# Kernel tuning notes

Measured on AMD Instinct MI355X. Metric: run time of the kernel, lower is better.

Reference implementation:

```python
import jax, jax.numpy as jnp
import numpy as np

INPUT_SIZE = 512
HIDDEN = 1024
OUT = 512
LN_EPS = 1e-5


def setup_inputs() -> dict:
    key = jax.random.key(0)
    ks = jax.random.split(key, 12)
    B, T = 128, 512
    def lin(k, fan_in, shape):
        bound = 1.0 / np.sqrt(fan_in)
        return jax.random.uniform(k, shape, jnp.float32, -bound, bound)
    in0 = INPUT_SIZE + HIDDEN
    in1 = HIDDEN + HIDDEN
    return {
        "x": jax.random.normal(ks[0], (B, T, INPUT_SIZE), jnp.float32),
        "W0": lin(ks[1], in0, (in0, 4 * HIDDEN)),
        "b0": lin(ks[2], in0, (4 * HIDDEN,)),
        "g0": jnp.ones((4 * HIDDEN,), jnp.float32),
        "beta0": jnp.zeros((4 * HIDDEN,), jnp.float32),
        "W1": lin(ks[3], in1, (in1, 4 * HIDDEN)),
        "b1": lin(ks[4], in1, (4 * HIDDEN,)),
        "g1": jnp.ones((4 * HIDDEN,), jnp.float32),
        "beta1": jnp.zeros((4 * HIDDEN,), jnp.float32),
        "fcW": lin(ks[5], HIDDEN, (HIDDEN, OUT)),
        "fcb": lin(ks[6], HIDDEN, (OUT,)),
    }


def _layer_norm(z, g, b):
    m = jnp.mean(z, axis=-1, keepdims=True)
    v = jnp.mean((z - m) ** 2, axis=-1, keepdims=True)
    return (z - m) * jax.lax.rsqrt(v + LN_EPS) * g + b


def _cell(xin, h, c, W, b, g, beta):
    comb = jnp.concatenate([xin, h], axis=-1)          # [B, in+H]
    gates = _layer_norm(comb @ W + b, g, beta)          # [B, 4H]
    i, f, gg, o = jnp.split(gates, 4, axis=-1)
    i, f, o = jax.nn.sigmoid(i), jax.nn.sigmoid(f), jax.nn.sigmoid(o)
    gg = jnp.tanh(gg)
    c_new = f * c + i * gg
    h_new = o * jnp.tanh(c_new)
    return h_new, c_new


def reference(x, W0, b0, g0, beta0, W1, b1, g1, beta1, fcW, fcb):
    B = x.shape[0]
    params = [(W0, b0, g0, beta0), (W1, b1, g1, beta1)]
    h0 = tuple(jnp.zeros((B, HIDDEN), x.dtype) for _ in range(2))
    c0 = tuple(jnp.zeros((B, HIDDEN), x.dtype) for _ in range(2))

    def step(carry, xt):
        hs, cs = carry
        inp = xt
        new_h, new_c = [], []
        for l, (W, b, g, beta) in enumerate(params):
            hl, cl = _cell(inp, hs[l], cs[l], W, b, g, beta)
            new_h.append(hl)
            new_c.append(cl)
            inp = hl
        return (tuple(new_h), tuple(new_c)), None

    xt = jnp.swapaxes(x, 0, 1)  # [T, B, D]
    (hs, _), _ = jax.lax.scan(step, (h0, c0), xt)
    return hs[-1] @ fcW + fcb  # [B, OUT]
```

## Files before the change

### kernel.cpp

```cpp
#include <hip/hip_runtime.h>
#include <hip/hip_bf16.h>

typedef __attribute__((ext_vector_type(8))) _Float16 half8_t;
typedef __attribute__((ext_vector_type(4))) float f32x4_t;
typedef unsigned long long u64;

#define SH 2056
#define HMOFF (16 * SH)
#define LDS_BYTES (2 * 16 * SH * 2)

__device__ __forceinline__ float sigm(float z) { return 1.0f / (1.0f + __expf(-z)); }
__device__ __forceinline__ float tanh_fast(float z) {
  float e = __expf(2.0f * z);
  return 1.0f - 2.0f / (e + 1.0f);
}

__device__ __forceinline__ half8_t ld_h8_coh(const _Float16* p) {
  union { half8_t h; u64 q[2]; } r;
  u64* q = (u64*)p;
  r.q[0] = __hip_atomic_load(q,     __ATOMIC_RELAXED, __HIP_MEMORY_SCOPE_SYSTEM);
  r.q[1] = __hip_atomic_load(q + 1, __ATOMIC_RELAXED, __HIP_MEMORY_SCOPE_SYSTEM);
  return r.h;
}
__device__ __forceinline__ void st_h_coh(_Float16* p, _Float16 v) {
  unsigned short b = __builtin_bit_cast(unsigned short, v);
  __hip_atomic_store((unsigned short*)p, b, __ATOMIC_RELAXED, __HIP_MEMORY_SCOPE_SYSTEM);
}
__device__ __forceinline__ float ld_f_coh(const float* p) {
  return __hip_atomic_load((float*)p, __ATOMIC_RELAXED, __HIP_MEMORY_SCOPE_SYSTEM);
}
__device__ __forceinline__ void st_f_coh(float* p, float v) {
  __hip_atomic_store(p, v, __ATOMIC_RELAXED, __HIP_MEMORY_SCOPE_SYSTEM);
}


__global__ void lstm_prep(const float* __restrict__ W0, const float* __restrict__ W1,
                          const float* __restrict__ b0, const float* __restrict__ g0,
                          const float* __restrict__ be0, const float* __restrict__ b1,
                          const float* __restrict__ g1, const float* __restrict__ be1,
                          _Float16* __restrict__ W0a, _Float16* __restrict__ W0b,
                          _Float16* __restrict__ W1a, _Float16* __restrict__ W1b,
                          float* __restrict__ vecs)
{
  int gid = blockIdx.x * 256 + threadIdx.x;
  const int W0N = 192 * 4096;
  const int W1N = 256 * 4096;
  if (gid < W0N) {
    int k8 = gid >> 12, gp = gid & 4095;
    int colgrp = gp >> 7, w = (gp >> 4) & 7, c = gp & 15;
    int gcol = ((c >> 2) << 10) + (colgrp << 5) + (w << 2) + (c & 3);
    half8_t va, vb;
    #pragma unroll
    for (int j = 0; j < 8; ++j) {
      float w32 = W0[(size_t)(k8 * 8 + j) * 4096 + gcol] * 32.0f;
      _Float16 p1 = (_Float16)w32;
      float r = w32 - (float)p1;
      va[j] = p1; vb[j] = (_Float16)(r * 2048.0f);
    }
    *(half8_t*)&W0a[(size_t)gp * 1536 + k8 * 8] = va;
    *(half8_t*)&W0b[(size_t)gp * 1536 + k8 * 8] = vb;
  } else if (gid < W0N + W1N) {
    int g2 = gid - W0N;
    int k8 = g2 >> 12, gp = g2 & 4095;
    int colgrp = gp >> 7, w = (gp >> 4) & 7, c = gp & 15;
    int gcol = ((c >> 2) << 10) + (colgrp << 5) + (w << 2) + (c & 3);
    half8_t va, vb;
    #pragma unroll
    for (int j = 0; j < 8; ++j) {
      float w32 = W1[(size_t)(k8 * 8 + j) * 4096 + gcol] * 32.0f;
      _Float16 p1 = (_Float16)w32;
      float r = w32 - (float)p1;
      va[j] = p1; vb[j] = (_Float16)(r * 2048.0f);
    }
    *(half8_t*)&W1a[(size_t)gp * 2048 + k8 * 8] = va;
    *(half8_t*)&W1b[(size_t)gp * 2048 + k8 * 8] = vb;
  } else if (gid < W0N + W1N + 6 * 4096) {
    int g2 = gid - W0N - W1N;
    int j = g2 >> 12, gp = g2 & 4095;
    int colgrp = gp >> 7, w = (gp >> 4) & 7, c = gp & 15;
    int gcol = ((c >> 2) << 10) + (colgrp << 5) + (w << 2) + (c & 3);
    const float* src = (j == 0) ? b0 : (j == 1) ? g0 : (j == 2) ? be0
                     : (j == 3) ? b1 : (j == 4) ? g1 : be1;
    vecs[j * 4096 + gp] = src[gcol];
  }
}

#define MFMA16(A, B, C) __builtin_amdgcn_mfma_f32_16x16x32_f16(A, B, C, 0, 0, 0)

__device__ __forceinline__ void gridbar(unsigned* bars, int wgid, int tid, unsigned ep) {
  __syncthreads();
  if (tid == 0) {
    const int q = ep & 1;
    unsigned old = __hip_atomic_fetch_add(&bars[(q * 8 + (wgid & 7)) * 32], 1u,
                                          __ATOMIC_RELAXED, __HIP_MEMORY_SCOPE_AGENT);
    if (old == 31u) {
      unsigned mo = __hip_atomic_fetch_add(&bars[512 + q * 32], 1u,
                                           __ATOMIC_RELAXED, __HIP_MEMORY_SCOPE_AGENT);
      if (mo == 7u) {
        #pragma unroll
        for (int g = 0; g < 8; ++g)
          __hip_atomic_store(&bars[(q * 8 + g) * 32], 0u, __ATOMIC_RELAXED, __HIP_MEMORY_SCOPE_SYSTEM);
        __hip_atomic_store(&bars[512 + q * 32], 0u, __ATOMIC_RELAXED, __HIP_MEMORY_SCOPE_SYSTEM);
        __hip_atomic_store(&bars[576], ep, __ATOMIC_RELEASE, __HIP_MEMORY_SCOPE_SYSTEM);
      }
    }
    while (__hip_atomic_load(&bars[576], __ATOMIC_RELAXED, __HIP_MEMORY_SCOPE_SYSTEM) < ep) {}
  }
  __syncthreads();
}

__global__ void __launch_bounds__(512, 2) lstm_seq(
    const float* __restrict__ x,
    const _Float16* __restrict__ W0ap,
    const _Float16* __restrict__ W0bp,
    const _Float16* __restrict__ W1ap,
    const _Float16* __restrict__ W1bp,
    const float* __restrict__ vecs,
    _Float16* __restrict__ hch,
    _Float16* __restrict__ hcm,
    float* __restrict__ stats,
    unsigned* __restrict__ bars,
    const float* __restrict__ fcW,
    const float* __restrict__ fcb,
    float* __restrict__ out)
{
  extern __shared__ _Float16 hS[];
  const int tid = threadIdx.x;
  const int wgid = blockIdx.x;
  const int mtile = wgid >> 5;
  const int colgrp = wgid & 31;
  const int wid = tid >> 6;
  const int lane = tid & 63;
  const int c16 = lane & 15;
  const int klo = lane >> 4;
  const int rowbase = mtile * 16;

  const int gp = colgrp * 128 + wid * 16 + c16;
  const float b0v  = vecs[gp];
  const float g0v  = vecs[4096 + gp];
  const float be0v = vecs[8192 + gp];
  const float b1v  = vecs[12288 + gp];
  const float g1v  = vecs[16384 + gp];
  const float be1v = vecs[20480 + gp];

  const int arow = rowbase + c16;
  const float* xbase = x + (size_t)arow * 512 * 512;
  const _Float16* w0a = W0ap + (size_t)gp * 1536;
  const _Float16* w0b = W0bp + (size_t)gp * 1536;
  const _Float16* w1a = W1ap + (size_t)gp * 2048;
  const _Float16* w1b = W1bp + (size_t)gp * 2048;
  const int repbase = (wgid & 15) << 2;
  const int cbase = colgrp * 32 + wid * 4;

  float c0s[4] = {0,0,0,0};
  float c1s[4] = {0,0,0,0};
  unsigned ep = 0;
  half8_t stg[16];

#define STAGE_ISSUE() {                                                       \
    _Pragma("unroll")                                                         \
    for (int j = 0; j < 16; ++j) {                                            \
      int linear = tid + 512 * j;                                             \
      int plane = linear >> 12;                                               \
      int rem = linear & 4095;                                                \
      int row = rem >> 8;                                                     \
      int ck  = rem & 255;                                                    \
      const _Float16* srcp = (plane ? hcm : hch)                              \
                           + (size_t)(rowbase + row) * 2048 + ck * 8;         \
      stg[j] = ld_h8_coh(srcp);                                               \
    } }

#define STAGE_COMMIT() {                                                      \
    _Pragma("unroll")                                                         \
    for (int j = 0; j < 16; ++j) {                                            \
      int linear = tid + 512 * j;                                             \
      int plane = linear >> 12;                                               \
      int rem = linear & 4095;                                                \
      int row = rem >> 8;                                                     \
      int ck  = rem & 255;                                                    \
      *(half8_t*)&hS[plane * HMOFF + row * SH + ck * 8] = stg[j];             \
    }                                                                         \
    __syncthreads(); }

#define SPLIT2(E, J) { float e_ = (E); _Float16 h1_ = (_Float16)e_;           \
  float r_ = e_ - (float)h1_; ah[J] = h1_; am[J] = (_Float16)(r_ * 2048.0f); }

#define PROD3(HA, MA) \
  HA = MFMA16(ah, bh0, HA);                                                   \
  MA = MFMA16(ah, bm0, MA);                                                   \
  MA = MFMA16(am, bh0, MA);

#define X_BODY(KB, HA, MA) {                                                  \
      float4 xu = *(const float4*)(xp + (KB) * 32);                           \
      float4 xw = *(const float4*)(xp + (KB) * 32 + 4);                       \
      half8_t ah, am;                                                         \
      SPLIT2(xu.x, 0) SPLIT2(xu.y, 1) SPLIT2(xu.z, 2) SPLIT2(xu.w, 3)         \
      SPLIT2(xw.x, 4) SPLIT2(xw.y, 5) SPLIT2(xw.z, 6) SPLIT2(xw.w, 7)         \
      half8_t bh0 = *(const half8_t*)&w0a[(KB) * 32 + klo * 8];               \
      half8_t bm0 = *(const half8_t*)&w0b[(KB) * 32 + klo * 8];               \
      PROD3(HA, MA) }

#define H0_BODY(KB, HA, MA) {                                                 \
      half8_t ah = *(const half8_t*)&hS[c16 * SH + (KB) * 32 + klo * 8];      \
      half8_t am = *(const half8_t*)&hS[HMOFF + c16 * SH + (KB) * 32 + klo * 8]; \
      half8_t bh0 = *(const half8_t*)&w0a[512 + (KB) * 32 + klo * 8];         \
      half8_t bm0 = *(const half8_t*)&w0b[512 + (KB) * 32 + klo * 8];         \
      PROD3(HA, MA) }

#define H1_BODY(KB, HA, MA) {                                                 \
      half8_t ah = *(const half8_t*)&hS[c16 * SH + (KB) * 32 + klo * 8];      \
      half8_t am = *(const half8_t*)&hS[HMOFF + c16 * SH + (KB) * 32 + klo * 8]; \
      half8_t bh0 = *(const half8_t*)&w1a[(KB) * 32 + klo * 8];               \
      half8_t bm0 = *(const half8_t*)&w1b[(KB) * 32 + klo * 8];               \
      PROD3(HA, MA) }

#define STAT_ADD(V, BUF) {                                                    \
    _Pragma("unroll")                                                         \
    for (int r = 0; r < 4; ++r) {                                             \
      float s = V[r];                                                         \
      float q = V[r]*V[r];                                                    \
      _Pragma("unroll")                                                       \
      for (int m = 1; m <= 8; m <<= 1) { s += __shfl_xor(s, m); q += __shfl_xor(q, m); } \
      if (c16 == 0) {                                                         \
        int row = rowbase + klo * 4 + r;                                      \
        atomicAdd(&stats[(repbase + (BUF)) * 256 + row * 2 + 0], s);          \
        atomicAdd(&stats[(repbase + (BUF)) * 256 + row * 2 + 1], q);          \
      }                                                                       \
    } }

#define CELL(V, BUF, CS, GC, BEC, HB) {                                       \
    _Pragma("unroll")                                                         \
    for (int r = 0; r < 4; ++r) {                                             \
      int row = rowbase + klo * 4 + r;                                        \
      const float* sp = stats + ((c16 << 2) + (BUF)) * 256 + row * 2;         \
      float s_ = ld_f_coh(sp), q_ = ld_f_coh(sp + 1);                         \
      _Pragma("unroll")                                                       \
      for (int m = 1; m <= 8; m <<= 1) { s_ += __shfl_xor(s_, m); q_ += __shfl_xor(q_, m); } \
      float mean = s_ * (1.0f / 4096.0f);                                     \
      float msq  = q_ * (1.0f / 4096.0f);                                     \
      float rstd = rsqrtf(msq - mean * mean + 1e-5f);                         \
      float gh = (V[r] - mean) * rstd * GC + BEC;                             \
      float fg = __shfl_down(gh, 4);                                          \
      float gg = __shfl_down(gh, 8);                                          \
      float og = __shfl_down(gh, 12);                                         \
      if (c16 < 4) {                                                          \
        float iv = sigm(gh), fv = sigm(fg), zv = tanh_fast(gg), ov = sigm(og); \
        float cc = fv * CS[r] + iv * zv;                                      \
        CS[r] = cc;                                                           \
        float hv = ov * tanh_fast(cc);                                        \
        int idx = row * 2048 + (HB) + cbase + c16;                            \
        _Float16 h1v = (_Float16)hv;                                          \
        st_h_coh(&hch[idx], h1v);                                             \
        st_h_coh(&hcm[idx], (_Float16)((hv - (float)h1v) * 2048.0f));         \
      }                                                                       \
    } }

  f32x4_t ahe, aho, ame, amo;
  f32x4_t dhe, dho, dme, dmo;
  f32x4_t a0, d0;

#define A0_X(TT) {                                                            \
    ahe = {0,0,0,0}; aho = {0,0,0,0}; ame = {0,0,0,0}; amo = {0,0,0,0};       \
    const float* xp = xbase + (size_t)(TT) * 512 + klo * 8;                   \
    _Pragma("unroll 2")                                                       \
    for (int kb = 0; kb < 16; kb += 2) {                                      \
      X_BODY(kb,     ahe, ame);                                               \
      X_BODY(kb + 1, aho, amo);                                               \
    } }

#define A0_H0() {                                                             \
    _Pragma("unroll 2")                                                       \
    for (int kb = 0; kb < 32; kb += 2) {                                      \
      H0_BODY(kb,     ahe, ame);                                              \
      H0_BODY(kb + 1, aho, amo);                                              \
    }                                                                         \
    a0 = (ahe + aho) * 0.03125f + (ame + amo) * (1.0f / 65536.0f);            \
    _Pragma("unroll")                                                         \
    for (int r_ = 0; r_ < 4; ++r_) a0[r_] += b0v; }

  STAGE_ISSUE();
  STAGE_COMMIT();
  A0_X(0);
  A0_H0();
  STAT_ADD(a0, 0);
  gridbar(bars, wgid, tid, ++ep);
  CELL(a0, 0, c0s, g0v, be0v, 0);
  gridbar(bars, wgid, tid, ++ep);

  for (int t = 0; t < 512; ++t) {
    const int par = t & 1;
    const int npar = 1 - par;

    STAGE_ISSUE();
    if (t < 511) {
      A0_X(t + 1);
    }
    STAGE_COMMIT();

    dhe = {0,0,0,0}; dho = {0,0,0,0}; dme = {0,0,0,0}; dmo = {0,0,0,0};
    #pragma unroll 2
    for (int kb = 0; kb < 64; kb += 2) {
      H1_BODY(kb,     dhe, dme);
      H1_BODY(kb + 1, dho, dmo);
    }
    d0 = (dhe + dho) * 0.03125f + (dme + dmo) * (1.0f / 65536.0f);
    #pragma unroll
    for (int r = 0; r < 4; ++r) d0[r] += b1v;
    STAT_ADD(d0, 2 + par);

    if (t < 511) {
      A0_H0();
      STAT_ADD(a0, npar);
    }

    {
      int rep2 = ((wgid & 7) << 1) + (tid >> 8);
      int ent  = tid & 255;
      if (wgid < 8)       st_f_coh(&stats[((rep2 << 2) + 2 + npar) * 256 + ent], 0.0f);
      else if (wgid < 16) st_f_coh(&stats[((rep2 << 2) + par) * 256 + ent], 0.0f);
    }

    gridbar(bars, wgid, tid, ++ep);

    CELL(d0, 2 + par, c1s, g1v, be1v, 1024);
    if (t < 511) {
      CELL(a0, npar, c0s, g0v, be0v, 0);
    }
    gridbar(bars, wgid, tid, ++ep);
  }

  {
    int gid = wgid * 512 + tid;
    if (gid < 65536) {
      int b = gid >> 9, o = gid & 511;
      const _Float16* p1 = hch + (size_t)b * 2048 + 1024;
      const _Float16* p2 = hcm + (size_t)b * 2048 + 1024;
      float s = fcb[o];
      #pragma unroll 4
      for (int k = 0; k < 1024; k += 4) {
        union { u64 q; _Float16 h[4]; } ua, um;
        ua.q = __hip_atomic_load((u64*)(p1 + k), __ATOMIC_RELAXED, __HIP_MEMORY_SCOPE_SYSTEM);
        um.q = __hip_atomic_load((u64*)(p2 + k), __ATOMIC_RELAXED, __HIP_MEMORY_SCOPE_SYSTEM);
        #pragma unroll
        for (int i = 0; i < 4; ++i) {
          float h = (float)ua.h[i] + (float)um.h[i] * (1.0f / 2048.0f);
          s = fmaf(h, fcW[(k + i) * 512 + o], s);
        }
      }
      out[gid] = s;
    }
  }
}

extern "C" void kernel_launch(void* const* d_in, const int* in_sizes, int n_in,
                              void* d_out, int out_size, void* d_ws, size_t ws_size,
                              hipStream_t stream) {
  const float* x   = (const float*)d_in[0];
  const float* W0  = (const float*)d_in[1];
  const float* b0  = (const float*)d_in[2];
  const float* g0  = (const float*)d_in[3];
  const float* be0 = (const float*)d_in[4];
  const float* W1  = (const float*)d_in[5];
  const float* b1  = (const float*)d_in[6];
  const float* g1  = (const float*)d_in[7];
  const float* be1 = (const float*)d_in[8];
  const float* fcW = (const float*)d_in[9];
  const float* fcb = (const float*)d_in[10];
  float* out = (float*)d_out;

  char* ws = (char*)d_ws;
  _Float16* W0a  = (_Float16*)(ws);
  _Float16* W0b  = (_Float16*)(ws + 12582912);
  _Float16* W1a  = (_Float16*)(ws + 25165824);
  _Float16* W1b  = (_Float16*)(ws + 41943040);
  float* vecs    = (float*)(ws + 58720256);
  _Float16* hch  = (_Float16*)(ws + 58818560);
  _Float16* hcm  = (_Float16*)(ws + 59342848);
  float* stats   = (float*)(ws + 59867136);
  unsigned* bars = (unsigned*)(ws + 59932672);

  hipMemsetAsync(hch, 0, 524288 + 524288 + 65536 + 8192, stream);
  lstm_prep<<<7264, 256, 0, stream>>>(W0, W1, b0, g0, be0, b1, g1, be1,
                                      W0a, W0b, W1a, W1b, vecs);

  hipFuncSetAttribute((const void*)lstm_seq,
                      hipFuncAttributeMaxDynamicSharedMemorySize, LDS_BYTES);
  void* args[] = { (void*)&x, (void*)&W0a, (void*)&W0b, (void*)&W1a, (void*)&W1b,
                   (void*)&vecs, (void*)&hch, (void*)&hcm,
                   (void*)&stats, (void*)&bars,
                   (void*)&fcW, (void*)&fcb, (void*)&out };
  hipError_t lerr = hipLaunchCooperativeKernel((const void*)lstm_seq,
                                               dim3(256), dim3(512),
                                               args, LDS_BYTES, stream);
  if (lerr != hipSuccess) {
    (void)hipGetLastError();
    lstm_seq<<<dim3(256), dim3(512), LDS_BYTES, stream>>>(
        x, W0a, W0b, W1a, W1b, vecs, hch, hcm, stats, bars, fcW, fcb, out);
  }
}
```

Before: 37.86 ms.

## Replace grid-wide barrier with per-batch-tile group barriers and interleave H0/H1 MFMA loops

Batch rows are independent in the LSTM recurrence, so the global two-level barrier across all workgroups is replaced by barriers that only sync the 32 workgroups sharing a batch tile (mtile). Stats zeroing and the final FC output mapping are reassigned per group to match. The layer-0 hidden matmul is also interleaved into the layer-1 K loop to give more independent MFMA work per iteration. The risk is that the per-group indexing of stats and barriers must be correct, and the interleaving adds register pressure.

```diff
diff --git a/kernel.cpp b/kernel.cpp
--- a/kernel.cpp
+++ b/kernel.cpp
@@ -87,24 +87,17 @@
 
 #define MFMA16(A, B, C) __builtin_amdgcn_mfma_f32_16x16x32_f16(A, B, C, 0, 0, 0)
 
-__device__ __forceinline__ void gridbar(unsigned* bars, int wgid, int tid, unsigned ep) {
+__device__ __forceinline__ void groupbar(unsigned* bars, int grp, int tid, unsigned ep) {
   __syncthreads();
   if (tid == 0) {
     const int q = ep & 1;
-    unsigned old = __hip_atomic_fetch_add(&bars[(q * 8 + (wgid & 7)) * 32], 1u,
+    unsigned old = __hip_atomic_fetch_add(&bars[(grp * 2 + q) * 32], 1u,
                                           __ATOMIC_RELAXED, __HIP_MEMORY_SCOPE_AGENT);
     if (old == 31u) {
-      unsigned mo = __hip_atomic_fetch_add(&bars[512 + q * 32], 1u,
-                                           __ATOMIC_RELAXED, __HIP_MEMORY_SCOPE_AGENT);
-      if (mo == 7u) {
-        #pragma unroll
-        for (int g = 0; g < 8; ++g)
-          __hip_atomic_store(&bars[(q * 8 + g) * 32], 0u, __ATOMIC_RELAXED, __HIP_MEMORY_SCOPE_SYSTEM);
-        __hip_atomic_store(&bars[512 + q * 32], 0u, __ATOMIC_RELAXED, __HIP_MEMORY_SCOPE_SYSTEM);
-        __hip_atomic_store(&bars[576], ep, __ATOMIC_RELEASE, __HIP_MEMORY_SCOPE_SYSTEM);
-      }
-    }
-    while (__hip_atomic_load(&bars[576], __ATOMIC_RELAXED, __HIP_MEMORY_SCOPE_SYSTEM) < ep) {}
+      __hip_atomic_store(&bars[(grp * 2 + q) * 32], 0u, __ATOMIC_RELAXED, __HIP_MEMORY_SCOPE_SYSTEM);
+      __hip_atomic_store(&bars[1024 + grp * 32], ep, __ATOMIC_RELEASE, __HIP_MEMORY_SCOPE_SYSTEM);
+    }
+    while (__hip_atomic_load(&bars[1024 + grp * 32], __ATOMIC_RELAXED, __HIP_MEMORY_SCOPE_SYSTEM) < ep) {}
   }
   __syncthreads();
 }
@@ -149,7 +142,7 @@
   const _Float16* w0b = W0bp + (size_t)gp * 1536;
   const _Float16* w1a = W1ap + (size_t)gp * 2048;
   const _Float16* w1b = W1bp + (size_t)gp * 2048;
-  const int repbase = (wgid & 15) << 2;
+  const int repbase = (colgrp & 15) << 2;
   const int cbase = colgrp * 32 + wid * 4;
 
   float c0s[4] = {0,0,0,0};
@@ -268,12 +261,7 @@
       X_BODY(kb + 1, aho, amo);                                               \
     } }
 
-#define A0_H0() {                                                             \
-    _Pragma("unroll 2")                                                       \
-    for (int kb = 0; kb < 32; kb += 2) {                                      \
-      H0_BODY(kb,     ahe, ame);                                              \
-      H0_BODY(kb + 1, aho, amo);                                              \
-    }                                                                         \
+#define A0_COMBINE() {                                                        \
     a0 = (ahe + aho) * 0.03125f + (ame + amo) * (1.0f / 65536.0f);            \
     _Pragma("unroll")                                                         \
     for (int r_ = 0; r_ < 4; ++r_) a0[r_] += b0v; }
@@ -281,11 +269,16 @@
   STAGE_ISSUE();
   STAGE_COMMIT();
   A0_X(0);
-  A0_H0();
+  #pragma unroll 2
+  for (int kb = 0; kb < 32; kb += 2) {
+    H0_BODY(kb,     ahe, ame);
+    H0_BODY(kb + 1, aho, amo);
+  }
+  A0_COMBINE();
   STAT_ADD(a0, 0);
-  gridbar(bars, wgid, tid, ++ep);
+  groupbar(bars, mtile, tid, ++ep);
   CELL(a0, 0, c0s, g0v, be0v, 0);
-  gridbar(bars, wgid, tid, ++ep);
+  groupbar(bars, mtile, tid, ++ep);
 
   for (int t = 0; t < 512; ++t) {
     const int par = t & 1;
@@ -298,10 +291,22 @@
     STAGE_COMMIT();
 
     dhe = {0,0,0,0}; dho = {0,0,0,0}; dme = {0,0,0,0}; dmo = {0,0,0,0};
-    #pragma unroll 2
-    for (int kb = 0; kb < 64; kb += 2) {
-      H1_BODY(kb,     dhe, dme);
-      H1_BODY(kb + 1, dho, dmo);
+    if (t < 511) {
+      #pragma unroll 2
+      for (int i = 0; i < 32; i += 2) {
+        H1_BODY(2*i,     dhe, dme);
+        H1_BODY(2*i+1,   dho, dmo);
+        H0_BODY(i,       ahe, ame);
+        H1_BODY(2*i+2,   dhe, dme);
+        H1_BODY(2*i+3,   dho, dmo);
+        H0_BODY(i+1,     aho, amo);
+      }
+    } else {
+      #pragma unroll 2
+      for (int kb = 0; kb < 64; kb += 2) {
+        H1_BODY(kb,     dhe, dme);
+        H1_BODY(kb + 1, dho, dmo);
+      }
     }
     d0 = (dhe + dho) * 0.03125f + (dme + dmo) * (1.0f / 65536.0f);
     #pragma unroll
@@ -309,30 +314,28 @@
     STAT_ADD(d0, 2 + par);
 
     if (t < 511) {
-      A0_H0();
+      A0_COMBINE();
       STAT_ADD(a0, npar);
     }
 
-    {
-      int rep2 = ((wgid & 7) << 1) + (tid >> 8);
-      int ent  = tid & 255;
-      if (wgid < 8)       st_f_coh(&stats[((rep2 << 2) + 2 + npar) * 256 + ent], 0.0f);
-      else if (wgid < 16) st_f_coh(&stats[((rep2 << 2) + par) * 256 + ent], 0.0f);
-    }
-
-    gridbar(bars, wgid, tid, ++ep);
+    if (colgrp < 16 && tid < 64) {
+      int bufsel = ((tid >> 5) == 0) ? (2 + npar) : par;
+      st_f_coh(&stats[((colgrp << 2) + bufsel) * 256 + mtile * 32 + (tid & 31)], 0.0f);
+    }
+
+    groupbar(bars, mtile, tid, ++ep);
 
     CELL(d0, 2 + par, c1s, g1v, be1v, 1024);
     if (t < 511) {
       CELL(a0, npar, c0s, g0v, be0v, 0);
     }
-    gridbar(bars, wgid, tid, ++ep);
+    groupbar(bars, mtile, tid, ++ep);
   }
 
   {
-    int gid = wgid * 512 + tid;
-    if (gid < 65536) {
-      int b = gid >> 9, o = gid & 511;
+    if (tid < 256) {
+      int b = rowbase + (tid >> 4);
+      int o = colgrp * 16 + (tid & 15);
       const _Float16* p1 = hch + (size_t)b * 2048 + 1024;
       const _Float16* p2 = hcm + (size_t)b * 2048 + 1024;
       float s = fcb[o];
@@ -347,7 +350,7 @@
           s = fmaf(h, fcW[(k + i) * 512 + o], s);
         }
       }
-      out[gid] = s;
+      out[b * 512 + o] = s;
     }
   }
 }
```

Measured after the change: 36.77 ms. 1.03x faster.
